# Kernel optimization log

Measured on AMD Instinct MI355X. Metric: run time of the kernel, lower is better.

The kernel has to match this reference:

```python
import jax, jax.numpy as jnp
import numpy as np

N = 1_000_000
B, X, Y, Z = 2, 512, 512, 64
F_IN, H = 64, 32
SCORE_T = 0.1      # score_thres
CENT_T = 0.2       # centroid_thres
MAX_TREES = 64     # max_trees_per_scene
NEG = -1e30        # stand-in for -inf (inactive voxel sites)


def setup_inputs() -> dict:
    key = jax.random.key(0)
    ks = jax.random.split(key, 8)
    feats = jax.random.normal(ks[0], (N, F_IN), dtype=jnp.float32)
    cb = jax.random.randint(ks[1], (N,), 0, B, dtype=jnp.int32)
    cx = jax.random.randint(ks[2], (N,), 0, X, dtype=jnp.int32)
    cy = jax.random.randint(ks[3], (N,), 0, Y, dtype=jnp.int32)
    cz = jax.random.randint(ks[4], (N,), 0, Z, dtype=jnp.int32)
    mask = jax.random.randint(ks[5], (N,), 0, 2, dtype=jnp.int32) == 1
    # decoder params: Linear(64->32) + ReLU, Linear(32->1) with init bias
    W1 = jax.random.normal(ks[6], (F_IN, H), dtype=jnp.float32) * 0.1
    b1 = jnp.zeros((H,), dtype=jnp.float32)
    W2 = jax.random.normal(ks[7], (H, 1), dtype=jnp.float32) * 0.5
    b2 = jnp.full((1,), -1.0, dtype=jnp.float32)  # ~log(density/(1-density)), shifted so peaks exist
    return {"feats": feats, "cb": cb, "cx": cx, "cy": cy, "cz": cz,
            "mask": mask, "W1": W1, "b1": b1, "W2": W2, "b2": b2}


def reference(feats, cb, cx, cy, cz, mask, W1, b1, W2, b2):
    # --- FeatDecoder (pointwise MLP over sparse voxel features) + sigmoid ---
    h = jax.nn.relu(feats @ W1 + b1)                 # [N, 32]
    score = jax.nn.sigmoid(h @ W2 + b2)              # [N, 1]
    score = jnp.where(mask[:, None], score, 0.0)     # decoder only applied on masked voxels
    s = score[:, 0]

    # --- _find_centroid_peaks: submanifold 3x3x3 sparse max pool over candidates ---
    cand = s > SCORE_T                                # score-threshold mask
    # scatter candidate scores into a padded dense grid (inactive sites = NEG)
    grid = jnp.full((B, X + 2, Y + 2, Z + 2), NEG, dtype=jnp.float32)
    grid = grid.at[cb, cx + 1, cy + 1, cz + 1].max(jnp.where(cand, s, NEG))
    # gather all 27 neighbors per voxel and take the max (submanifold pool, pad=1)
    off = jnp.arange(-1, 2)
    dx, dy, dz = [a.ravel() for a in jnp.meshgrid(off, off, off, indexing='ij')]  # [27]
    nb = grid[cb[:, None], cx[:, None] + 1 + dx[None, :],
              cy[:, None] + 1 + dy[None, :], cz[:, None] + 1 + dz[None, :]]       # [N, 27]
    hmax = nb.max(axis=1)

    # peak = local max among candidates AND above centroid threshold
    peak = cand & (hmax == s) & (s > CENT_T)

    # top-k selection, fixed size max_trees_per_scene * batch_size (padded with -1 scores)
    max_peaks = MAX_TREES * B
    peak_scores, peak_indices = jax.lax.top_k(jnp.where(peak, s, -1.0), max_peaks)
    coords = jnp.stack([cb, cx, cy, cz], axis=1)      # [N, 4]
    peak_coords = coords[peak_indices]                # [max_peaks, 4]
    return score, peak_indices, peak_scores, peak_coords
```

## Files before the change

### kernel.cpp

```cpp
#include <hip/hip_runtime.h>
#include <stdint.h>

#define N_PTS 1000000
#define FIN   64
#define HID   32
#define GB    2
#define GX    512
#define GY    512
#define GZ    64
#define KMAX  128
#define NBUCKET 4096
#define BITS_LO 0x3E4CCCCDu
#define BUCKET_SHIFT 13
#define CAND_CAP 4096

#define BM_WORDS   (GB*GX*GY)
#define BM_BYTES   ((size_t)BM_WORDS*8)
#define HIST_OFF   BM_BYTES
#define HIST_BYTES (NBUCKET*4)
#define CNT_OFF    (HIST_OFF + HIST_BYTES)
#define CNT_BYTES  64
#define CLEAR_BYTES (CNT_OFF + CNT_BYTES)
#define GRID_OFF   ((size_t)4214784)
#define GRID_CELLS ((size_t)GB*GX*GY*GZ)
#define GRID_BYTES (GRID_CELLS*4)
#define KEYS_OFF   (GRID_OFF + GRID_BYTES)
#define CAND_OFF   (KEYS_OFF + (size_t)N_PTS*8)


__global__ __launch_bounds__(256) void k_mlp(
    const float* __restrict__ feats,
    const int* __restrict__ cb, const int* __restrict__ cx,
    const int* __restrict__ cy, const int* __restrict__ cz,
    const int* __restrict__ mask_i,
    const float* __restrict__ W1, const float* __restrict__ b1,
    const float* __restrict__ W2, const float* __restrict__ b2,
    float* __restrict__ score_out, int* __restrict__ grid,
    unsigned long long* __restrict__ bm)
{
    __shared__ unsigned int s_mflag;
    if (threadIdx.x == 0) s_mflag = 0u;
    __syncthreads();
    {
        unsigned int v = (unsigned int)mask_i[threadIdx.x];
        if (v > 1u) atomicOr(&s_mflag, 1u);
    }
    __syncthreads();
    bool mask_is_bytes = (s_mflag != 0u);

    int i = blockIdx.x * 256 + threadIdx.x;
    if (i >= N_PTS) return;

    bool mk = mask_is_bytes ? (((const unsigned char*)mask_i)[i] != 0)
                            : (mask_i[i] != 0);

    float s = 0.0f;
    if (mk) {
        float hj[HID];
#pragma unroll
        for (int j = 0; j < HID; ++j) hj[j] = b1[j];

        const float4* rp = (const float4*)(feats + (size_t)i * FIN);
#pragma unroll 4
        for (int q = 0; q < FIN / 4; ++q) {
            float4 v = rp[q];
            const float* w0 = W1 + (4*q + 0) * HID;
            const float* w1 = W1 + (4*q + 1) * HID;
            const float* w2 = W1 + (4*q + 2) * HID;
            const float* w3 = W1 + (4*q + 3) * HID;
#pragma unroll
            for (int j = 0; j < HID; ++j) {
                float acc = hj[j];
                acc = fmaf(v.x, w0[j], acc);
                acc = fmaf(v.y, w1[j], acc);
                acc = fmaf(v.z, w2[j], acc);
                acc = fmaf(v.w, w3[j], acc);
                hj[j] = acc;
            }
        }

        float x = b2[0];
#pragma unroll
        for (int j = 0; j < HID; ++j) x += fmaxf(hj[j], 0.0f) * W2[j];

        s = 1.0f / (1.0f + expf(-x));
    }

    score_out[i] = s;

    if (s > 0.1f) {
        int sb = (int)__float_as_uint(s);
        int b = cb[i], xx = cx[i], yy = cy[i], zz = cz[i];
        int col = (b*GX + xx)*GY + yy;
        atomicOr(&bm[col], 1ull << zz);
        atomicMax(&grid[((size_t)col << 6) + (size_t)zz], sb);
    }
}

__global__ __launch_bounds__(256) void k_peak(
    const float* __restrict__ s_buf,
    const int* __restrict__ cb, const int* __restrict__ cx,
    const int* __restrict__ cy, const int* __restrict__ cz,
    const int* __restrict__ grid,
    const unsigned long long* __restrict__ bm,
    unsigned long long* __restrict__ keys,
    unsigned int* __restrict__ hist)
{
    int i = blockIdx.x * 256 + threadIdx.x;
    if (i >= N_PTS) return;
    float s = s_buf[i];
    bool cand = (s > 0.2f);

    int  sb = (int)__float_as_uint(s);
    bool peak = false;
    unsigned int bucket = 0;

    if (cand) {
        int b = cb[i], x = cx[i], y = cy[i], z = cz[i];
        int z0 = (z > 0) ? z - 1 : 0;
        int z1 = (z < GZ-1) ? z + 1 : GZ-1;
        unsigned wmask = (1u << (z1 - z0 + 1)) - 1u;

        int xm = (x > 0) ? x - 1 : 0;
        int xp = (x < GX-1) ? x + 1 : GX-1;
        int ym = (y > 0) ? y - 1 : 0;
        int yp = (y < GY-1) ? y + 1 : GY-1;
        int rb = b * GX;
        int c0 = (rb + xm) * GY, c1 = (rb + x) * GY, c2 = (rb + xp) * GY;
        int col0 = c0+ym, col1 = c0+y, col2 = c0+yp;
        int col3 = c1+ym, col4 = c1+y, col5 = c1+yp;
        int col6 = c2+ym, col7 = c2+y, col8 = c2+yp;

        unsigned long long w0 = bm[col0], w1 = bm[col1], w2 = bm[col2];
        unsigned long long w3 = bm[col3], w4 = bm[col4], w5 = bm[col5];
        unsigned long long w6 = bm[col6], w7 = bm[col7], w8 = bm[col8];

        int vmax = (int)0x80000000;
#define CHK(WV, CL) do { \
            unsigned win = (unsigned)((WV) >> z0) & wmask; \
            while (win) { \
                int t = __ffs(win) - 1; win &= win - 1u; \
                int v = grid[((size_t)(CL) << 6) + (size_t)(z0 + t)]; \
                vmax = (v > vmax) ? v : vmax; \
            } \
        } while (0)
        CHK(w0, col0); CHK(w1, col1); CHK(w2, col2);
        CHK(w3, col3); CHK(w4, col4); CHK(w5, col5);
        CHK(w6, col6); CHK(w7, col7); CHK(w8, col8);
#undef CHK
        peak = (vmax <= sb);
        bucket = ((unsigned int)sb - BITS_LO) >> BUCKET_SHIFT;
        if (bucket > NBUCKET - 1u) bucket = NBUCKET - 1u;
    }

    unsigned long long kv = 0ull;
    if (peak) {
        kv = ((unsigned long long)(unsigned int)sb << 32) | (unsigned int)(~(unsigned int)i);
        atomicAdd(&hist[bucket], 1u);
    }
    keys[i] = kv;
}

__global__ __launch_bounds__(256) void k_collect(
    const unsigned long long* __restrict__ keys,
    unsigned long long* __restrict__ cand,
    unsigned int* __restrict__ counters,
    const unsigned int* __restrict__ hist)
{
    __shared__ unsigned int lh[NBUCKET];
    __shared__ unsigned int csum[256];
    __shared__ unsigned int s_cut;
    int t = threadIdx.x;
    if (t == 0) s_cut = 0u;
    unsigned int ssum = 0;
    for (int k = 0; k < NBUCKET/256; ++k) {
        unsigned int v = hist[t*(NBUCKET/256) + k];
        lh[t*(NBUCKET/256) + k] = v;
        ssum += v;
    }
    csum[t] = ssum;
    __syncthreads();
    for (int off = 1; off < 256; off <<= 1) {
        unsigned int v = (t + off < 256) ? csum[t + off] : 0u;
        __syncthreads();
        csum[t] += v;
        __syncthreads();
    }
    unsigned int incl = csum[t];
    unsigned int excl = (t + 1 < 256) ? csum[t + 1] : 0u;
    if (incl >= KMAX && excl < KMAX) {
        unsigned int cum = excl;
        int cut = t * (NBUCKET/256);
        for (int b = t*(NBUCKET/256) + (NBUCKET/256) - 1; b >= t*(NBUCKET/256); --b) {
            cum += lh[b];
            if (cum >= KMAX) { cut = b; break; }
        }
        s_cut = (unsigned int)cut;
    }
    __syncthreads();
    unsigned int cut = s_cut;

    for (unsigned int i = blockIdx.x * 256 + t; i < N_PTS; i += gridDim.x * 256) {
        unsigned long long k = keys[i];
        bool take = false;
        if (k != 0ull) {
            unsigned int sbu = (unsigned int)(k >> 32);
            unsigned int bucket = (sbu - BITS_LO) >> BUCKET_SHIFT;
            if (bucket > NBUCKET - 1u) bucket = NBUCKET - 1u;
            take = (bucket >= cut);
        }
        unsigned long long bal = __ballot(take ? 1 : 0);
        if (bal) {
            int lane = threadIdx.x & 63;
            int leader = __ffsll((long long)bal) - 1;
            unsigned int base = 0;
            if (lane == leader) base = atomicAdd(&counters[1], (unsigned int)__popcll(bal));
            base = __shfl(base, leader);
            if (take) {
                unsigned int p = base + (unsigned int)__popcll(bal & ((1ull << lane) - 1ull));
                if (p < CAND_CAP) cand[p] = k;
            }
        }
    }
}

__global__ __launch_bounds__(1024) void k_final(
    const unsigned long long* __restrict__ cand,
    const unsigned int* __restrict__ counters,
    const int* __restrict__ cb, const int* __restrict__ cx,
    const int* __restrict__ cy, const int* __restrict__ cz,
    float* __restrict__ out)
{
    __shared__ unsigned long long sk[CAND_CAP];
    int t = threadIdx.x;
    unsigned int C = counters[1];
    if (C > CAND_CAP) C = CAND_CAP;
    int P = KMAX;
    while (P < (int)C) P <<= 1;
    for (int k = t; k < P; k += 1024) sk[k] = (k < (int)C) ? cand[k] : 0ull;
    __syncthreads();

    for (int k = 2; k <= P; k <<= 1) {
        for (int j = k >> 1; j > 0; j >>= 1) {
            for (int i = t; i < P; i += 1024) {
                int ixj = i ^ j;
                if (ixj > i) {
                    unsigned long long a = sk[i], b = sk[ixj];
                    bool up = ((i & k) == 0);
                    if (up ? (a < b) : (a > b)) { sk[i] = b; sk[ixj] = a; }
                }
            }
            __syncthreads();
        }
    }

    if (t < KMAX) {
        unsigned long long k = sk[t];
        float val; int idx;
        if (k != 0ull) {
            idx = (int)(~(unsigned int)(k & 0xFFFFFFFFull));
            val = __uint_as_float((unsigned int)(k >> 32));
        } else {
            idx = t;
            val = -1.0f;
        }
        out[N_PTS + t]         = (float)idx;
        out[N_PTS + KMAX + t]  = val;
        float* pc = out + N_PTS + 2*KMAX + 4*t;
        pc[0] = (float)cb[idx]; pc[1] = (float)cx[idx];
        pc[2] = (float)cy[idx]; pc[3] = (float)cz[idx];
    }
}

extern "C" void kernel_launch(void* const* d_in, const int* in_sizes, int n_in,
                              void* d_out, int out_size, void* d_ws, size_t ws_size,
                              hipStream_t stream) {
    const float* feats = (const float*)d_in[0];
    const int*   cb    = (const int*)d_in[1];
    const int*   cx    = (const int*)d_in[2];
    const int*   cy    = (const int*)d_in[3];
    const int*   cz    = (const int*)d_in[4];
    const int*   mask  = (const int*)d_in[5];
    const float* W1    = (const float*)d_in[6];
    const float* b1    = (const float*)d_in[7];
    const float* W2    = (const float*)d_in[8];
    const float* b2    = (const float*)d_in[9];
    float* out = (float*)d_out;

    char* ws = (char*)d_ws;
    unsigned long long* bm       = (unsigned long long*)(ws);
    unsigned int*       hist     = (unsigned int*)(ws + HIST_OFF);
    unsigned int*       counters = (unsigned int*)(ws + CNT_OFF);
    int*                grid     = (int*)(ws + GRID_OFF);
    unsigned long long* keys     = (unsigned long long*)(ws + KEYS_OFF);
    unsigned long long* cand     = (unsigned long long*)(ws + CAND_OFF);

    hipMemsetAsync(ws, 0, CLEAR_BYTES, stream);

    int nb = (N_PTS + 255) / 256;
    k_mlp<<<nb, 256, 0, stream>>>(feats, cb, cx, cy, cz, mask,
                                  W1, b1, W2, b2, out, grid, bm);
    k_peak<<<nb, 256, 0, stream>>>(out, cb, cx, cy, cz, grid, bm, keys, hist);
    k_collect<<<512, 256, 0, stream>>>(keys, cand, counters, hist);
    k_final<<<1, 1024, 0, stream>>>(cand, counters, cb, cx, cy, cz, out);
}
```

Measured before the change: 443.6 us.

## Compact masked rows per block and stage features through shared memory for MLP

Each block uses wave ballots and a prefix count to compact the indices of masked points into a shared list. It then stages those feature rows into padded shared memory with coalesced float4 loads, so the active threads that run the MLP are contiguous and waves no longer diverge on the mask. Unmasked points get their zero score written up front. The cost is extra shared memory (about 35KB per block), which may limit occupancy, plus added barriers, and only about half the threads do the compute.

Result: slower. 466.7 us (+5.2%).

```diff
diff --git a/kernel.cpp b/kernel.cpp
--- a/kernel.cpp
+++ b/kernel.cpp
@@ -27,6 +27,9 @@
 #define KEYS_OFF   (GRID_OFF + GRID_BYTES)
 #define CAND_OFF   (KEYS_OFF + (size_t)N_PTS*8)
 
+#define MAXSTAGE  128
+#define ROWSTRIDE 68
+
 
 __global__ __launch_bounds__(256) void k_mlp(
     const float* __restrict__ feats,
@@ -39,61 +42,102 @@
     unsigned long long* __restrict__ bm)
 {
     __shared__ unsigned int s_mflag;
-    if (threadIdx.x == 0) s_mflag = 0u;
+    __shared__ int s_wcnt[4];
+    __shared__ unsigned char s_act[256];
+    __shared__ float sf[MAXSTAGE * ROWSTRIDE];
+
+    int t = threadIdx.x;
+
+    if (t == 0) s_mflag = 0u;
     __syncthreads();
     {
-        unsigned int v = (unsigned int)mask_i[threadIdx.x];
+        unsigned int v = (unsigned int)mask_i[t];
         if (v > 1u) atomicOr(&s_mflag, 1u);
     }
     __syncthreads();
     bool mask_is_bytes = (s_mflag != 0u);
 
-    int i = blockIdx.x * 256 + threadIdx.x;
-    if (i >= N_PTS) return;
-
-    bool mk = mask_is_bytes ? (((const unsigned char*)mask_i)[i] != 0)
-                            : (mask_i[i] != 0);
-
-    float s = 0.0f;
-    if (mk) {
-        float hj[HID];
+    int base = blockIdx.x * 256;
+    int i = base + t;
+    bool valid = (i < N_PTS);
+    bool mk = false;
+    if (valid)
+        mk = mask_is_bytes ? (((const unsigned char*)mask_i)[i] != 0)
+                           : (mask_i[i] != 0);
+
+    if (valid && !mk) score_out[i] = 0.0f;
+
+    int wave = t >> 6, lane = t & 63;
+    unsigned long long bal = __ballot(mk ? 1 : 0);
+    if (lane == 0) s_wcnt[wave] = (int)__popcll(bal);
+    __syncthreads();
+    int A = s_wcnt[0] + s_wcnt[1] + s_wcnt[2] + s_wcnt[3];
+    {
+        int pre = 0;
+        if (wave > 0) pre += s_wcnt[0];
+        if (wave > 1) pre += s_wcnt[1];
+        if (wave > 2) pre += s_wcnt[2];
+        if (mk) {
+            int pos = pre + (int)__popcll(bal & ((1ull << lane) - 1ull));
+            s_act[pos] = (unsigned char)t;
+        }
+    }
+    __syncthreads();
+
+    for (int p0 = 0; p0 < A; p0 += MAXSTAGE) {
+        int cnt = A - p0; if (cnt > MAXSTAGE) cnt = MAXSTAGE;
+
+        for (int n = t; n < cnt * 16; n += 256) {
+            int r = n >> 4, c = n & 15;
+            int row = (int)s_act[p0 + r];
+            float4 v = *((const float4*)(feats + (size_t)(base + row) * FIN) + c);
+            *(float4*)(&sf[r * ROWSTRIDE + c * 4]) = v;
+        }
+        __syncthreads();
+
+        if (t < cnt) {
+            int gi = base + (int)s_act[p0 + t];
+
+            float hj[HID];
 #pragma unroll
-        for (int j = 0; j < HID; ++j) hj[j] = b1[j];
-
-        const float4* rp = (const float4*)(feats + (size_t)i * FIN);
+            for (int j = 0; j < HID; ++j) hj[j] = b1[j];
+
+            const float* lf = &sf[t * ROWSTRIDE];
 #pragma unroll 4
-        for (int q = 0; q < FIN / 4; ++q) {
-            float4 v = rp[q];
-            const float* w0 = W1 + (4*q + 0) * HID;
-            const float* w1 = W1 + (4*q + 1) * HID;
-            const float* w2 = W1 + (4*q + 2) * HID;
-            const float* w3 = W1 + (4*q + 3) * HID;
+            for (int q = 0; q < FIN / 4; ++q) {
+                float4 v = *(const float4*)(lf + q * 4);
+                const float* w0 = W1 + (4*q + 0) * HID;
+                const float* w1 = W1 + (4*q + 1) * HID;
+                const float* w2 = W1 + (4*q + 2) * HID;
+                const float* w3 = W1 + (4*q + 3) * HID;
 #pragma unroll
-            for (int j = 0; j < HID; ++j) {
-                float acc = hj[j];
-                acc = fmaf(v.x, w0[j], acc);
-                acc = fmaf(v.y, w1[j], acc);
-                acc = fmaf(v.z, w2[j], acc);
-                acc = fmaf(v.w, w3[j], acc);
-                hj[j] = acc;
+                for (int j = 0; j < HID; ++j) {
+                    float acc = hj[j];
+                    acc = fmaf(v.x, w0[j], acc);
+                    acc = fmaf(v.y, w1[j], acc);
+                    acc = fmaf(v.z, w2[j], acc);
+                    acc = fmaf(v.w, w3[j], acc);
+                    hj[j] = acc;
+                }
             }
-        }
-
-        float x = b2[0];
+
+            float x = b2[0];
 #pragma unroll
-        for (int j = 0; j < HID; ++j) x += fmaxf(hj[j], 0.0f) * W2[j];
-
-        s = 1.0f / (1.0f + expf(-x));
-    }
-
-    score_out[i] = s;
-
-    if (s > 0.1f) {
-        int sb = (int)__float_as_uint(s);
-        int b = cb[i], xx = cx[i], yy = cy[i], zz = cz[i];
-        int col = (b*GX + xx)*GY + yy;
-        atomicOr(&bm[col], 1ull << zz);
-        atomicMax(&grid[((size_t)col << 6) + (size_t)zz], sb);
+            for (int j = 0; j < HID; ++j) x += fmaxf(hj[j], 0.0f) * W2[j];
+
+            float s = 1.0f / (1.0f + expf(-x));
+
+            score_out[gi] = s;
+
+            if (s > 0.1f) {
+                int sb = (int)__float_as_uint(s);
+                int b = cb[gi], xx = cx[gi], yy = cy[gi], zz = cz[gi];
+                int col = (b*GX + xx)*GY + yy;
+                atomicOr(&bm[col], 1ull << zz);
+                atomicMax(&grid[((size_t)col << 6) + (size_t)zz], sb);
+            }
+        }
+        __syncthreads();
     }
 }
 
```
